# Kernel tuning notes

Measured on AMD Instinct MI355X. Metric: run time of the kernel, lower is better.

The kernel has to match this reference:

```python
import jax, jax.numpy as jnp
import numpy as np

H = 32   # hidden_size
E = 64   # embed_size
L = 3    # gru num_layers
V = 258  # vocab (256 pixel values + 2 specials)
B, C, R, S = 16, 3, 64, 64


def setup_inputs() -> dict:
    key = jax.random.key(0)
    ks = jax.random.split(key, 18)
    sc = jnp.float32(0.15)
    f = lambda k, shp: (jax.random.normal(k, shp, dtype=jnp.float32) * sc)
    return {
        "x": jax.random.randint(ks[0], (B, C, R, S), 0, V),
        "target": jax.random.randint(ks[1], (B, C, R, S), 0, V),
        "emb": f(ks[2], (3, V, E)),
        "gru_Wih0": f(ks[3], (3, 3 * H, E + 1)),
        "gru_WihR": f(ks[4], (3, L - 1, 3 * H, H)),
        "gru_Whh": f(ks[5], (3, L, 3 * H, H)),
        "gru_bih": f(ks[6], (3, L, 3 * H)),
        "gru_bhh": f(ks[7], (3, L, 3 * H)),
        "h2e_W": f(ks[8], (3, E + 1, H)),
        "h2e_b": f(ks[9], (3, E + 1)),
        "adp_W": f(ks[10], (2, E + 1, H)),
        "adp_b": f(ks[11], (2, E + 1)),
        "red_W": f(ks[12], (V, H)),
        "red_b": f(ks[13], (V,)),
        "green_W": f(ks[14], (V, H + E)),
        "green_b": f(ks[15], (V,)),
        "blue_W": f(ks[16], (V, H + 2 * E)),
        "blue_b": f(ks[17], (V,)),
    }


def _gru(comb, Wih0, WihR, Whh, bih, bhh):
    # comb: (B, S, E+1). Multi-layer GRU over the col axis, zero initial hidden.
    # PyTorch gate order: r, z, n.
    b = comb.shape[0]
    h0 = jnp.zeros((L, b, H), comb.dtype)

    def step(h, x_t):
        inp = x_t
        hs = []
        for l in range(L):
            Wih = Wih0 if l == 0 else WihR[l - 1]
            gi = inp @ Wih.T + bih[l]
            gh = h[l] @ Whh[l].T + bhh[l]
            r = jax.nn.sigmoid(gi[:, :H] + gh[:, :H])
            z = jax.nn.sigmoid(gi[:, H:2 * H] + gh[:, H:2 * H])
            n = jnp.tanh(gi[:, 2 * H:] + r * gh[:, 2 * H:])
            hl = (1.0 - z) * n + z * h[l]
            hs.append(hl)
            inp = hl
        return jnp.stack(hs), inp  # output = top-layer hidden

    _, outs = jax.lax.scan(step, h0, jnp.swapaxes(comb, 0, 1))
    return jnp.swapaxes(outs, 0, 1)  # (B, S, H)


def _forward(x, target, emb, gru_Wih0, gru_WihR, gru_Whh, gru_bih, gru_bhh,
             h2e_W, h2e_b, adp_W, adp_b, red_W, red_b, green_W, green_b,
             blue_W, blue_b):
    b, _, r_, s_ = x.shape
    row_pos = ((jnp.arange(r_) / r_) * 2.0 - 1.0).astype(jnp.float32)
    row_feat = jnp.broadcast_to(row_pos[None, :, None, None], (b, r_, s_, 1))

    outs = []
    prev = None
    for c in range(3):
        ex = jnp.concatenate([emb[c][x[:, c]], row_feat], axis=-1)  # (B,R,S,E+1)
        if c > 0:
            xs = (jnp.swapaxes(ex, 0, 1), jnp.swapaxes(prev, 0, 1))
        else:
            xs = jnp.swapaxes(ex, 0, 1)

        def row_step(ph, xr, c=c):
            # ph: (B, S, H) = GRU output of previous row
            if c > 0:
                cur, po = xr
                comb = cur + ph @ h2e_W[c].T + h2e_b[c] + po @ adp_W[c - 1].T + adp_b[c - 1]
            else:
                comb = xr + ph @ h2e_W[c].T + h2e_b[c]
            g = _gru(comb, gru_Wih0[c], gru_WihR[c], gru_Whh[c], gru_bih[c], gru_bhh[c])
            return g, g

        _, o = jax.lax.scan(row_step, jnp.zeros((b, s_, H), jnp.float32), xs)
        o = jnp.swapaxes(o, 0, 1)  # (B, R, S, H)
        outs.append(o)
        prev = o

    red_logits = outs[0] @ red_W.T + red_b
    red_e = emb[0][target[:, 0]]
    green_logits = jnp.concatenate([outs[1], red_e], axis=-1) @ green_W.T + green_b
    green_e = emb[1][target[:, 1]]
    blue_logits = jnp.concatenate([outs[2], red_e, green_e], axis=-1) @ blue_W.T + blue_b
    return jnp.stack([red_logits, green_logits, blue_logits], axis=1)  # (B,3,R,S,V)


def reference(x, target, emb, gru_Wih0, gru_WihR, gru_Whh, gru_bih, gru_bhh,
              h2e_W, h2e_b, adp_W, adp_b, red_W, red_b, green_W, green_b,
              blue_W, blue_b):
    return _forward(x, target, emb, gru_Wih0, gru_WihR, gru_Whh, gru_bih,
                    gru_bhh, h2e_W, h2e_b, adp_W, adp_b, red_W, red_b,
                    green_W, green_b, blue_W, blue_b)
```

## Files before the change

### kernel.cpp

```cpp
#include <hip/hip_runtime.h>
#include <hip/hip_bf16.h>

using bf16 = __hip_bfloat16;
typedef __attribute__((ext_vector_type(8))) short bfrag;
typedef __attribute__((ext_vector_type(4))) float ffrag;

constexpr int kH  = 32;
constexpr int kE  = 64;
constexpr int kV  = 258;
constexpr int kB  = 16;
constexpr int kR  = 64;
constexpr int kS  = 64;
constexpr int kG  = 96;
constexpr int kEP = 65;

constexpr int H2_OFF   = (3*kB*kR*kS*kH)/2;
constexpr int PROG_OFF = H2_OFF;
constexpr int T_OFF    = H2_OFF + kB*kR*kH;
constexpr int WPH_OFF  = T_OFF + 3*kV*kG;
constexpr int WADP_OFF = WPH_OFF + 3*kG*kH;
constexpr int C0_OFF   = WADP_OFF + 2*kG*kH;
constexpr int RW_OFF   = C0_OFF + 3*kG;
constexpr int TG_OFF   = RW_OFF + 3*kG;
constexpr int TBR_OFF  = TG_OFF + kV*kV;
constexpr int TBG_OFF  = TBR_OFF + kV*kV;
constexpr int P_EMB    = TBG_OFF + kV*kV;
constexpr int P_WIH0   = P_EMB    + 3*kV*kE;
constexpr int P_WIHR   = P_WIH0   + 3*kG*kEP;
constexpr int P_WHH    = P_WIHR   + 3*2*kG*kH;
constexpr int P_BIH    = P_WHH    + 3*3*kG*kH;
constexpr int P_BHH    = P_BIH    + 3*3*kG;
constexpr int P_H2EW   = P_BHH    + 3*3*kG;
constexpr int P_H2EB   = P_H2EW   + 3*kEP*kH;
constexpr int P_ADPW   = P_H2EB   + 3*kEP;
constexpr int P_ADPB   = P_ADPW   + 2*kEP*kH;
constexpr int P_REDW   = P_ADPB   + 2*kEP;
constexpr int P_REDB   = P_REDW   + kV*kH;
constexpr int P_GREENW = P_REDB   + kV;
constexpr int P_GREENB = P_GREENW + kV*(kH+kE);
constexpr int P_BLUEW  = P_GREENB + kV;
constexpr int P_BLUEB  = P_BLUEW  + kV*(kH+2*kE);
constexpr int WS_END   = P_BLUEB  + kV;

__device__ __forceinline__ float tof(bf16 h) { return __bfloat162float(h); }

__device__ __forceinline__ unsigned short bfbits(bf16 h) {
  union { bf16 h; unsigned short u; } cv; cv.h = h; return cv.u;
}
__device__ __forceinline__ short f2b(float v) {
  return (short)bfbits(__float2bfloat16(v));
}
__device__ __forceinline__ float b2f(short s) {
  union { unsigned short u; } cv; cv.u = (unsigned short)s;
  bf16 h; __builtin_memcpy(&h, &cv.u, 2); return __bfloat162float(h);
}
__device__ __forceinline__ float sigm(float v) { return 1.0f / (1.0f + __expf(-v)); }
__device__ __forceinline__ float tanh_(float v) { return 1.0f - 2.0f / (__expf(2.0f * v) + 1.0f); }

#define MFMA16(a, bb, cc) __builtin_amdgcn_mfma_f32_16x16x32_bf16((a), (bb), (cc), 0, 0, 0)

__device__ __forceinline__ void lds_barrier() {
  __builtin_amdgcn_sched_barrier(0);
  asm volatile("s_waitcnt lgkmcnt(0)" ::: "memory");
  __builtin_amdgcn_s_barrier();
  __builtin_amdgcn_sched_barrier(0);
}

__global__ void norm_kernel(const void* p0, const void* p1, const void* p2, const void* p3,
                            const void* p4, const void* p5, const void* p6, const void* p7,
                            const void* p8, const void* p9, const void* p10, const void* p11,
                            const void* p12, const void* p13, const void* p14, const void* p15,
                            float* __restrict__ wsf)
{
  constexpr int counts[16] = {3*kV*kE, 3*kG*kEP, 3*2*kG*kH, 3*3*kG*kH, 3*3*kG, 3*3*kG,
                              3*kEP*kH, 3*kEP, 2*kEP*kH, 2*kEP, kV*kH, kV,
                              kV*(kH+kE), kV, kV*(kH+2*kE), kV};
  constexpr int dsts[16] = {P_EMB, P_WIH0, P_WIHR, P_WHH, P_BIH, P_BHH,
                            P_H2EW, P_H2EB, P_ADPW, P_ADPB, P_REDW, P_REDB,
                            P_GREENW, P_GREENB, P_BLUEW, P_BLUEB};
  const void* srcs[16] = {p0,p1,p2,p3,p4,p5,p6,p7,p8,p9,p10,p11,p12,p13,p14,p15};

  __shared__ unsigned int smax;
  const int a = blockIdx.x;
  const void* src = srcs[a];
  const int n = counts[a];
  if (threadIdx.x == 0) smax = 0;
  if (a == 0) {
    int* prog = (int*)(wsf + PROG_OFF);
    for (int i = threadIdx.x; i < 48; i += 256) prog[i] = 0;
  }
  __syncthreads();

  const unsigned short* u16 = (const unsigned short*)src;
  const int ns = (n < 2048) ? n : 2048;
  unsigned int lm = 0;
  for (int i = threadIdx.x; i < ns; i += 256) {
    unsigned int e = ((unsigned int)u16[i] >> 7) & 0xFFu;
    if (e > lm) lm = e;
  }
  atomicMax(&smax, lm);
  __syncthreads();

  const bool isf32 = (smax >= 135);
  float* dst = wsf + dsts[a];
  if (isf32) {
    const float* s = (const float*)src;
    for (int i = threadIdx.x; i < n; i += 256) dst[i] = s[i];
  } else {
    const bf16* s = (const bf16*)src;
    for (int i = threadIdx.x; i < n; i += 256) dst[i] = tof(s[i]);
  }
}

__global__ void prep_kernel(float* __restrict__ wsf)
{
  int idx = blockIdx.x * 256 + threadIdx.x;

  if (idx < 3*kV*kG) {
    int c = idx / (kV*kG);
    int rem = idx - c*(kV*kG);
    int v = rem / kG;
    int j = rem - v*kG;
    const float* ev = wsf + P_EMB + (c*kV + v)*kE;
    const float* wr = wsf + P_WIH0 + (c*kG + j)*kEP;
    float acc = 0.f;
    for (int e = 0; e < kE; ++e) acc = fmaf(ev[e], wr[e], acc);
    wsf[T_OFF + idx] = acc;
    return;
  }
  idx -= 3*kV*kG;

  if (idx < 3*kG*kH) {
    int c = idx / (kG*kH);
    int rem = idx - c*(kG*kH);
    int j = rem >> 5;
    int k = rem & 31;
    const float* wr = wsf + P_WIH0 + (c*kG + j)*kEP;
    const float* hw = wsf + P_H2EW + c*kEP*kH + k;
    float acc = 0.f;
    for (int e = 0; e < kEP; ++e) acc = fmaf(wr[e], hw[e*kH], acc);
    wsf[WPH_OFF + idx] = acc;
    return;
  }
  idx -= 3*kG*kH;

  if (idx < 2*kG*kH) {
    int cm = idx / (kG*kH);
    int rem = idx - cm*(kG*kH);
    int j = rem >> 5;
    int k = rem & 31;
    const float* wr = wsf + P_WIH0 + ((cm+1)*kG + j)*kEP;
    const float* aw = wsf + P_ADPW + cm*kEP*kH + k;
    float acc = 0.f;
    for (int e = 0; e < kEP; ++e) acc = fmaf(wr[e], aw[e*kH], acc);
    wsf[WADP_OFF + idx] = acc;
    return;
  }
  idx -= 2*kG*kH;

  if (idx < 3*kG) {
    int c = idx / kG;
    int j = idx - c*kG;
    const float* wr = wsf + P_WIH0 + (c*kG + j)*kEP;
    float acc = wsf[P_BIH + (c*3 + 0)*kG + j];
    for (int e = 0; e < kEP; ++e) acc = fmaf(wsf[P_H2EB + c*kEP + e], wr[e], acc);
    if (c > 0)
      for (int e = 0; e < kEP; ++e) acc = fmaf(wsf[P_ADPB + (c-1)*kEP + e], wr[e], acc);
    wsf[C0_OFF + idx] = acc;
    return;
  }
  idx -= 3*kG;

  if (idx < 3*kG) {
    int c = idx / kG;
    int j = idx - c*kG;
    wsf[RW_OFF + idx] = wsf[P_WIH0 + (c*kG + j)*kEP + kE];
    return;
  }
  idx -= 3*kG;

  if (idx < kV*kV) {
    int v = idx / kV, w = idx - (idx / kV)*kV;
    const float* ev = wsf + P_EMB + v*kE;
    const float* gw = wsf + P_GREENW + w*(kH + kE) + kH;
    float acc = 0.f;
    for (int e = 0; e < kE; ++e) acc = fmaf(ev[e], gw[e], acc);
    wsf[TG_OFF + idx] = acc;
    return;
  }
  idx -= kV*kV;

  if (idx < kV*kV) {
    int v = idx / kV, w = idx - (idx / kV)*kV;
    const float* ev = wsf + P_EMB + v*kE;
    const float* bw = wsf + P_BLUEW + w*(kH + 2*kE) + kH;
    float acc = 0.f;
    for (int e = 0; e < kE; ++e) acc = fmaf(ev[e], bw[e], acc);
    wsf[TBR_OFF + idx] = acc;
    return;
  }
  idx -= kV*kV;

  if (idx < kV*kV) {
    int v = idx / kV, w = idx - (idx / kV)*kV;
    const float* ev = wsf + P_EMB + (kV + v)*kE;
    const float* bw = wsf + P_BLUEW + w*(kH + 2*kE) + kH + kE;
    float acc = 0.f;
    for (int e = 0; e < kE; ++e) acc = fmaf(ev[e], bw[e], acc);
    wsf[TBG_OFF + idx] = acc;
  }
}

__global__ void tfold_kernel(float* __restrict__ wsf)
{
  int idx = blockIdx.x * 256 + threadIdx.x;
  if (idx >= 3*kV*kG) return;
  int c = idx / (kV*kG);
  int g = idx % kG;
  float add = wsf[C0_OFF + c*kG + g];
  if (g < 2*kH) add += wsf[P_BHH + (c*3 + 0)*kG + g];
  wsf[T_OFF + idx] += add;
}

__global__ __launch_bounds__(256, 1)
void recur_all_kernel(const int* __restrict__ x, float* __restrict__ wsf)
{
  __shared__ __align__(16) short RING[2][kR][kH];
  __shared__ __align__(16) short H0L[kR][kH];
  __shared__ __align__(16) short H1L[kR][kH];

  const int wg = blockIdx.x;
  const int c  = wg >> 4;
  const int b  = wg & 15;
  const int tid = threadIdx.x;
  const int w    = tid >> 6;
  const int lane = tid & 63;
  const int m    = lane & 15;
  const int q    = lane >> 4;
  const int ln   = m;
  const int cb0  = w * 16;

  for (int i = tid; i < 2*kR*kH; i += 256) (&RING[0][0][0])[i] = 0;
  for (int i = tid; i < kR*kH;   i += 256) (&H0L[0][0])[i] = 0;
  for (int i = tid; i < kR*kH;   i += 256) (&H1L[0][0])[i] = 0;

  const float* wsrc[7];
  wsrc[0] = wsf + WPH_OFF + c*kG*kH;
  wsrc[1] = wsf + P_WHH  + (c*3+0)*kG*kH;
  wsrc[2] = wsf + P_WIHR + (c*2+0)*kG*kH;
  wsrc[3] = wsf + P_WHH  + (c*3+1)*kG*kH;
  wsrc[4] = wsf + P_WIHR + (c*2+1)*kG*kH;
  wsrc[5] = wsf + P_WHH  + (c*3+2)*kG*kH;
  wsrc[6] = (c > 0) ? (wsf + WADP_OFF + (c-1)*kG*kH) : (wsf + WPH_OFF);
  bfrag Wb[7][6];
#pragma unroll
  for (int mt = 0; mt < 7; ++mt) {
#pragma unroll
    for (int u = 0; u < 6; ++u) {
      const float* p = wsrc[mt] + (u*16 + ln)*kH + q*8;
#pragma unroll
      for (int j = 0; j < 8; ++j) Wb[mt][u][j] = f2b(p[j]);
    }
  }

  float rwt[6], bh0n[2], bi1z[4], bi1n[2], bh1n[2], bi2z[4], bi2n[2], bh2n[2];
#pragma unroll
  for (int u = 0; u < 6; ++u) rwt[u] = wsf[RW_OFF + c*kG + u*16 + ln];
#pragma unroll
  for (int u = 0; u < 4; ++u) {
    int g = u*16 + ln;
    bi1z[u] = wsf[P_BIH + (c*3+1)*kG + g] + wsf[P_BHH + (c*3+1)*kG + g];
    bi2z[u] = wsf[P_BIH + (c*3+2)*kG + g] + wsf[P_BHH + (c*3+2)*kG + g];
  }
#pragma unroll
  for (int t2 = 0; t2 < 2; ++t2) {
    int g = 64 + t2*16 + ln;
    bh0n[t2] = wsf[P_BHH + (c*3+0)*kG + g];
    bi1n[t2] = wsf[P_BIH + (c*3+1)*kG + g];
    bh1n[t2] = wsf[P_BHH + (c*3+1)*kG + g];
    bi2n[t2] = wsf[P_BIH + (c*3+2)*kG + g];
    bh2n[t2] = wsf[P_BHH + (c*3+2)*kG + g];
  }

  float h0s[8], h1s[8], h2s[8];
#pragma unroll
  for (int i = 0; i < 8; ++i) { h0s[i] = 0.f; h1s[i] = 0.f; h2s[i] = 0.f; }

  unsigned short* outsAll = (unsigned short*)wsf;
  unsigned short* outsC = outsAll + (size_t)(c*kB + b) * (kR*kS*kH);
  const unsigned short* outsP = outsAll + (size_t)(((c > 0 ? c : 1) - 1)*kB + b) * (kR*kS*kH);
  int* prog = (int*)(wsf + PROG_OFF);
  const int* xc = x + (b*3 + c) * kR * kS;
  const float* Tc = wsf + T_OFF + (size_t)c * kV * kG;

  int rr0[4]; float rpw[4];
#pragma unroll
  for (int i = 0; i < 4; ++i) {
    rr0[i] = cb0 + q*4 + i;
    rpw[i] = (float)rr0[i] * (2.0f/64.0f) - 1.0f;
  }

  float tv[6][4];
  bfrag poPre;
  auto load_tv = [&](int dd) {
#pragma unroll
    for (int i = 0; i < 4; ++i) {
      int sv = dd - rr0[i];
      int scl = sv < 0 ? 0 : (sv > 63 ? 63 : sv);
      int xiv = xc[rr0[i]*kS + scl];
      const float* tp = Tc + (size_t)xiv*kG;
#pragma unroll
      for (int u = 0; u < 6; ++u) tv[u][i] = tp[u*16 + ln];
    }
  };
  auto load_po = [&](int dd) {
    int sv = dd - (cb0 + m);
    int scl = sv < 0 ? 0 : (sv > 63 ? 63 : sv);
    poPre = *(const bfrag*)&outsP[((size_t)(cb0 + m)*kS + scl)*kH + q*8];
  };
  load_tv(cb0);
#pragma unroll
  for (int j = 0; j < 8; ++j) poPre[j] = 0;

  __syncthreads();

  constexpr int DELTA = 4;
  constexpr int TT = (kR + kS - 1) + 2*DELTA;
  for (int t = 0; t < TT; ++t) {
    const int d = t - c*DELTA;

    if (tid == 0) {
      if (c < 2 && d >= 1 && d <= 127)
        __hip_atomic_store(&prog[c*16 + b], d, __ATOMIC_RELEASE, __HIP_MEMORY_SCOPE_AGENT);
      if (c > 0 && d >= -1 && d <= 125) {
        const int need = d + 2;
        while (__hip_atomic_load(&prog[(c-1)*16 + b], __ATOMIC_ACQUIRE,
                                 __HIP_MEMORY_SCOPE_AGENT) < need) { }
      }
    }
    lds_barrier();

    const bool activ = (d >= cb0) && (d <= cb0 + 78);
    if (activ) {
      const int ps = (d - 1) & 1;
      const int cs = d & 1;

      int ssv[4];
      bool act[4];
#pragma unroll
      for (int i = 0; i < 4; ++i) {
        ssv[i] = d - rr0[i];
        act[i] = ((unsigned)ssv[i]) < 64u;
      }
      const int row = cb0 + m;

      bfrag phA, h0A;
      {
        int pr = row - 1;
        int prc = pr < 0 ? 0 : pr;
        phA = *(const bfrag*)&RING[ps][prc][q*8];
        if (pr < 0) {
#pragma unroll
          for (int j = 0; j < 8; ++j) phA[j] = 0;
        }
        h0A = *(const bfrag*)&H0L[row][q*8];
      }
      bfrag poA = poPre;

      ffrag rz[4], gn[2], hn[2];
#pragma unroll
      for (int u = 0; u < 4; ++u)
#pragma unroll
        for (int i = 0; i < 4; ++i) rz[u][i] = 0.f;
#pragma unroll
      for (int t2 = 0; t2 < 2; ++t2)
#pragma unroll
        for (int i = 0; i < 4; ++i) { gn[t2][i] = 0.f; hn[t2][i] = bh0n[t2]; }

#pragma unroll
      for (int u = 0; u < 4; ++u)
        rz[u] = MFMA16(phA, Wb[0][u], rz[u]);
#pragma unroll
      for (int t2 = 0; t2 < 2; ++t2)
        gn[t2] = MFMA16(phA, Wb[0][4+t2], gn[t2]);
      if (c > 0) {
#pragma unroll
        for (int u = 0; u < 4; ++u)
          rz[u] = MFMA16(poA, Wb[6][u], rz[u]);
#pragma unroll
        for (int t2 = 0; t2 < 2; ++t2)
          gn[t2] = MFMA16(poA, Wb[6][4+t2], gn[t2]);
      }
#pragma unroll
      for (int u = 0; u < 4; ++u)
        rz[u] = MFMA16(h0A, Wb[1][u], rz[u]);
#pragma unroll
      for (int t2 = 0; t2 < 2; ++t2)
        hn[t2] = MFMA16(h0A, Wb[1][4+t2], hn[t2]);

#pragma unroll
      for (int u = 0; u < 4; ++u)
#pragma unroll
        for (int i = 0; i < 4; ++i) rz[u][i] += tv[u][i] + rpw[i]*rwt[u];
#pragma unroll
      for (int t2 = 0; t2 < 2; ++t2)
#pragma unroll
        for (int i = 0; i < 4; ++i) gn[t2][i] += tv[4+t2][i] + rpw[i]*rwt[4+t2];

      if (d + 1 <= cb0 + 78) {
        load_tv(d + 1);
        if (c > 0) load_po(d + 1);
      }

#pragma unroll
      for (int i = 0; i < 4; ++i)
#pragma unroll
        for (int th = 0; th < 2; ++th) {
          float rg = sigm(rz[th][i]);
          float zg = sigm(rz[2+th][i]);
          float ng = tanh_(gn[th][i] + rg*hn[th][i]);
          float h0v = (1.f - zg)*ng + zg*h0s[i*2+th];
          if (act[i]) {
            h0s[i*2+th] = h0v;
            H0L[rr0[i]][th*16 + ln] = f2b(h0v);
          }
        }
      bfrag h0An = *(const bfrag*)&H0L[row][q*8];

      bfrag h1A = *(const bfrag*)&H1L[row][q*8];
      ffrag rz1[4], gn1[2], hn1[2];
#pragma unroll
      for (int u = 0; u < 4; ++u)
#pragma unroll
        for (int i = 0; i < 4; ++i) rz1[u][i] = bi1z[u];
#pragma unroll
      for (int t2 = 0; t2 < 2; ++t2)
#pragma unroll
        for (int i = 0; i < 4; ++i) { gn1[t2][i] = bi1n[t2]; hn1[t2][i] = bh1n[t2]; }
#pragma unroll
      for (int u = 0; u < 4; ++u) {
        rz1[u] = MFMA16(h0An, Wb[2][u], rz1[u]);
        rz1[u] = MFMA16(h1A,  Wb[3][u], rz1[u]);
      }
#pragma unroll
      for (int t2 = 0; t2 < 2; ++t2) {
        gn1[t2] = MFMA16(h0An, Wb[2][4+t2], gn1[t2]);
        hn1[t2] = MFMA16(h1A,  Wb[3][4+t2], hn1[t2]);
      }
#pragma unroll
      for (int i = 0; i < 4; ++i)
#pragma unroll
        for (int th = 0; th < 2; ++th) {
          float rg = sigm(rz1[th][i]);
          float zg = sigm(rz1[2+th][i]);
          float ng = tanh_(gn1[th][i] + rg*hn1[th][i]);
          float h1v = (1.f - zg)*ng + zg*h1s[i*2+th];
          if (act[i]) {
            h1s[i*2+th] = h1v;
            H1L[rr0[i]][th*16 + ln] = f2b(h1v);
          }
        }
      bfrag h1An = *(const bfrag*)&H1L[row][q*8];

      bfrag h2A = *(const bfrag*)&RING[ps][row][q*8];
      if (m == d - cb0) {
#pragma unroll
        for (int j = 0; j < 8; ++j) h2A[j] = 0;
      }
      ffrag rz2[4], gn2[2], hn2[2];
#pragma unroll
      for (int u = 0; u < 4; ++u)
#pragma unroll
        for (int i = 0; i < 4; ++i) rz2[u][i] = bi2z[u];
#pragma unroll
      for (int t2 = 0; t2 < 2; ++t2)
#pragma unroll
        for (int i = 0; i < 4; ++i) { gn2[t2][i] = bi2n[t2]; hn2[t2][i] = bh2n[t2]; }
#pragma unroll
      for (int u = 0; u < 4; ++u) {
        rz2[u] = MFMA16(h1An, Wb[4][u], rz2[u]);
        rz2[u] = MFMA16(h2A,  Wb[5][u], rz2[u]);
      }
#pragma unroll
      for (int t2 = 0; t2 < 2; ++t2) {
        gn2[t2] = MFMA16(h1An, Wb[4][4+t2], gn2[t2]);
        hn2[t2] = MFMA16(h2A,  Wb[5][4+t2], hn2[t2]);
      }
#pragma unroll
      for (int i = 0; i < 4; ++i)
#pragma unroll
        for (int th = 0; th < 2; ++th) {
          float rg = sigm(rz2[th][i]);
          float zg = sigm(rz2[2+th][i]);
          float ng = tanh_(gn2[th][i] + rg*hn2[th][i]);
          float h2old = (ssv[i] == 0) ? 0.f : h2s[i*2+th];
          float h2v = (1.f - zg)*ng + zg*h2old;
          if (act[i]) {
            h2s[i*2+th] = h2v;
            short hb = f2b(h2v);
            RING[cs][rr0[i]][th*16 + ln] = hb;
            outsC[((size_t)rr0[i]*kS + ssv[i])*kH + th*16 + ln] = (unsigned short)hb;
          }
        }
    } else {
      if (d + 1 >= cb0 && d + 1 <= cb0 + 78) {
        load_tv(d + 1);
        if (c > 0) load_po(d + 1);
      }
    }

    if (c < 2) {
      __builtin_amdgcn_sched_barrier(0);
      asm volatile("s_waitcnt vmcnt(0)" ::: "memory");
    }
    lds_barrier();
  }
}

__global__ __launch_bounds__(256, 1)
void logits_kernel(const int* __restrict__ target, const float* __restrict__ wsf,
                   float* __restrict__ out)
{
  const int bx = blockIdx.x;
  const int ch = bx >> 10;
  const int b  = (bx >> 6) & 15;
  const int r  = bx & 63;

  const int tid  = threadIdx.x;
  const int wave = tid >> 6;
  const int lane = tid & 63;
  const int ln   = lane & 15;
  const int q    = lane >> 4;

  const int s0  = wave * 16;
  const int rsb = r * 64 + s0;

  const unsigned short* outsAll = (const unsigned short*)wsf;
  const unsigned short* hvp = outsAll + (size_t)(ch*kB + b)*(kR*kS*kH)
                                      + (size_t)(rsb + ln)*kH + q*8;
  bfrag hvA = *(const bfrag*)hvp;

  int trv[4], tgv[4];
  if (ch >= 1) {
    const int* tgt0 = target + (b*3 + 0)*4096;
#pragma unroll
    for (int i = 0; i < 4; ++i) trv[i] = tgt0[rsb + q*4 + i];
  }
  if (ch == 2) {
    const int* tgt1 = target + (b*3 + 1)*4096;
#pragma unroll
    for (int i = 0; i < 4; ++i) tgv[i] = tgt1[rsb + q*4 + i];
  }

  const float* wbase; const float* bbase; int wstride;
  if (ch == 0)      { wbase = wsf + P_REDW;   bbase = wsf + P_REDB;   wstride = kH; }
  else if (ch == 1) { wbase = wsf + P_GREENW; bbase = wsf + P_GREENB; wstride = kH + kE; }
  else              { wbase = wsf + P_BLUEW;  bbase = wsf + P_BLUEB;  wstride = kH + 2*kE; }

  const size_t obase = ((size_t)(b*3 + ch)*4096 + rsb);
  const float* TGt  = wsf + TG_OFF;
  const float* TBRt = wsf + TBR_OFF;
  const float* TBGt = wsf + TBG_OFF;

#pragma unroll
  for (int t = 0; t < 17; ++t) {
    const int v0 = t * 16;
    const int vr = v0 + ln;
    const int vv = (vr < kV) ? vr : (kV - 1);

    bfrag whi, wlo;
    {
      const float* wrow = wbase + (size_t)vv*wstride + q*8;
#pragma unroll
      for (int j = 0; j < 8; ++j) {
        float wv = wrow[j];
        short hi = f2b(wv);
        whi[j] = hi;
        wlo[j] = f2b(wv - b2f(hi));
      }
    }

    float bias = bbase[vv];
    ffrag acc;
#pragma unroll
    for (int i = 0; i < 4; ++i) {
      float a = bias;
      if (ch == 1)      a += TGt[(size_t)trv[i]*kV + vv];
      else if (ch == 2) a += TBRt[(size_t)trv[i]*kV + vv] + TBGt[(size_t)tgv[i]*kV + vv];
      acc[i] = a;
    }

    acc = MFMA16(hvA, wlo, acc);
    acc = MFMA16(hvA, whi, acc);

    if (vr < kV) {
#pragma unroll
      for (int i = 0; i < 4; ++i)
        out[(obase + q*4 + i)*kV + vr] = acc[i];
    }
  }
}

extern "C" void kernel_launch(void* const* d_in, const int* in_sizes, int n_in,
                              void* d_out, int out_size, void* d_ws, size_t ws_size,
                              hipStream_t stream)
{
  const int* x      = (const int*)d_in[0];
  const int* target = (const int*)d_in[1];
  float* wsf = (float*)d_ws;

  norm_kernel<<<16, 256, 0, stream>>>(d_in[2], d_in[3], d_in[4], d_in[5], d_in[6], d_in[7],
                                      d_in[8], d_in[9], d_in[10], d_in[11], d_in[12], d_in[13],
                                      d_in[14], d_in[15], d_in[16], d_in[17], wsf);
  const int prepN = 3*kV*kG + 3*kG*kH + 2*kG*kH + 3*kG + 3*kG + 3*kV*kV;
  prep_kernel<<<(prepN + 255)/256, 256, 0, stream>>>(wsf);
  tfold_kernel<<<(3*kV*kG + 255)/256, 256, 0, stream>>>(wsf);
  recur_all_kernel<<<48, 256, 0, stream>>>(x, wsf);
  logits_kernel<<<3*16*64, 256, 0, stream>>>(target, wsf, (float*)d_out);
}
```

Measured before the change: 1.197 ms.

## Pack two batches per recurrent block, drop trailing barrier, pipeline prefetch, fast rcp

```diff
diff --git a/kernel.cpp b/kernel.cpp
--- a/kernel.cpp
+++ b/kernel.cpp
@@ -54,8 +54,11 @@
   union { unsigned short u; } cv; cv.u = (unsigned short)s;
   bf16 h; __builtin_memcpy(&h, &cv.u, 2); return __bfloat162float(h);
 }
-__device__ __forceinline__ float sigm(float v) { return 1.0f / (1.0f + __expf(-v)); }
-__device__ __forceinline__ float tanh_(float v) { return 1.0f - 2.0f / (__expf(2.0f * v) + 1.0f); }
+__device__ __forceinline__ float frcp(float x) {
+  float r; asm("v_rcp_f32 %0, %1" : "=v"(r) : "v"(x)); return r;
+}
+__device__ __forceinline__ float sigm(float v) { return frcp(1.0f + __expf(-v)); }
+__device__ __forceinline__ float tanh_(float v) { return 1.0f - 2.0f*frcp(__expf(2.0f*v) + 1.0f); }
 
 #define MFMA16(a, bb, cc) __builtin_amdgcn_mfma_f32_16x16x32_bf16((a), (bb), (cc), 0, 0, 0)
 
@@ -222,27 +225,30 @@
   wsf[T_OFF + idx] += add;
 }
 
-__global__ __launch_bounds__(256, 1)
+__global__ __launch_bounds__(512, 2)
 void recur_all_kernel(const int* __restrict__ x, float* __restrict__ wsf)
 {
-  __shared__ __align__(16) short RING[2][kR][kH];
-  __shared__ __align__(16) short H0L[kR][kH];
-  __shared__ __align__(16) short H1L[kR][kH];
+  __shared__ __align__(16) short RING[2][2][kR][kH];
+  __shared__ __align__(16) short H0L[2][kR][kH];
+  __shared__ __align__(16) short H1L[2][kR][kH];
 
   const int wg = blockIdx.x;
-  const int c  = wg >> 4;
-  const int b  = wg & 15;
-  const int tid = threadIdx.x;
-  const int w    = tid >> 6;
+  const int c  = wg >> 3;
+  const int p  = wg & 7;
+  const int tid  = threadIdx.x;
+  const int half = tid >> 8;
+  const int b    = p*2 + half;
+  const int t2   = tid & 255;
+  const int w    = t2 >> 6;
   const int lane = tid & 63;
   const int m    = lane & 15;
   const int q    = lane >> 4;
   const int ln   = m;
   const int cb0  = w * 16;
 
-  for (int i = tid; i < 2*kR*kH; i += 256) (&RING[0][0][0])[i] = 0;
-  for (int i = tid; i < kR*kH;   i += 256) (&H0L[0][0])[i] = 0;
-  for (int i = tid; i < kR*kH;   i += 256) (&H1L[0][0])[i] = 0;
+  for (int i = tid; i < 2*2*kR*kH; i += 512) (&RING[0][0][0][0])[i] = 0;
+  for (int i = tid; i < 2*kR*kH;   i += 512) (&H0L[0][0][0])[i] = 0;
+  for (int i = tid; i < 2*kR*kH;   i += 512) (&H1L[0][0][0])[i] = 0;
 
   const float* wsrc[7];
   wsrc[0] = wsf + WPH_OFF + c*kG*kH;
@@ -257,9 +263,9 @@
   for (int mt = 0; mt < 7; ++mt) {
 #pragma unroll
     for (int u = 0; u < 6; ++u) {
-      const float* p = wsrc[mt] + (u*16 + ln)*kH + q*8;
-#pragma unroll
-      for (int j = 0; j < 8; ++j) Wb[mt][u][j] = f2b(p[j]);
+      const float* pp = wsrc[mt] + (u*16 + ln)*kH + q*8;
+#pragma unroll
+      for (int j = 0; j < 8; ++j) Wb[mt][u][j] = f2b(pp[j]);
     }
   }
 
@@ -273,13 +279,13 @@
     bi2z[u] = wsf[P_BIH + (c*3+2)*kG + g] + wsf[P_BHH + (c*3+2)*kG + g];
   }
 #pragma unroll
-  for (int t2 = 0; t2 < 2; ++t2) {
-    int g = 64 + t2*16 + ln;
-    bh0n[t2] = wsf[P_BHH + (c*3+0)*kG + g];
-    bi1n[t2] = wsf[P_BIH + (c*3+1)*kG + g];
-    bh1n[t2] = wsf[P_BHH + (c*3+1)*kG + g];
-    bi2n[t2] = wsf[P_BIH + (c*3+2)*kG + g];
-    bh2n[t2] = wsf[P_BHH + (c*3+2)*kG + g];
+  for (int s2 = 0; s2 < 2; ++s2) {
+    int g = 64 + s2*16 + ln;
+    bh0n[s2] = wsf[P_BHH + (c*3+0)*kG + g];
+    bi1n[s2] = wsf[P_BIH + (c*3+1)*kG + g];
+    bh1n[s2] = wsf[P_BHH + (c*3+1)*kG + g];
+    bi2n[s2] = wsf[P_BIH + (c*3+2)*kG + g];
+    bh2n[s2] = wsf[P_BHH + (c*3+2)*kG + g];
   }
 
   float h0s[8], h1s[8], h2s[8];
@@ -301,26 +307,51 @@
   }
 
   float tv[6][4];
+  int   xin[4];
   bfrag poPre;
-  auto load_tv = [&](int dd) {
+  const int d0 = -c*4;
+  {
 #pragma unroll
     for (int i = 0; i < 4; ++i) {
-      int sv = dd - rr0[i];
+      int sv = d0 - rr0[i];
       int scl = sv < 0 ? 0 : (sv > 63 ? 63 : sv);
-      int xiv = xc[rr0[i]*kS + scl];
-      const float* tp = Tc + (size_t)xiv*kG;
-#pragma unroll
-      for (int u = 0; u < 6; ++u) tv[u][i] = tp[u*16 + ln];
+      xin[i] = xc[rr0[i]*kS + scl];
+    }
+#pragma unroll
+    for (int i = 0; i < 4; ++i) {
+      const float* tp = Tc + (size_t)xin[i]*kG;
+#pragma unroll
+      for (int u = 0; u < 6; ++u) tv[u][i] = tp[u*16 + ln] + rpw[i]*rwt[u];
+    }
+#pragma unroll
+    for (int i = 0; i < 4; ++i) {
+      int sv = d0 + 1 - rr0[i];
+      int scl = sv < 0 ? 0 : (sv > 63 ? 63 : sv);
+      xin[i] = xc[rr0[i]*kS + scl];
+    }
+#pragma unroll
+    for (int j = 0; j < 8; ++j) poPre[j] = 0;
+  }
+
+  auto do_prefetch = [&](int d) {
+#pragma unroll
+    for (int i = 0; i < 4; ++i) {
+      const float* tp = Tc + (size_t)xin[i]*kG;
+#pragma unroll
+      for (int u = 0; u < 6; ++u) tv[u][i] = tp[u*16 + ln] + rpw[i]*rwt[u];
+    }
+#pragma unroll
+    for (int i = 0; i < 4; ++i) {
+      int sv = d + 2 - rr0[i];
+      int scl = sv < 0 ? 0 : (sv > 63 ? 63 : sv);
+      xin[i] = xc[rr0[i]*kS + scl];
+    }
+    {
+      int sv = d + 1 - (cb0 + m);
+      int scl = sv < 0 ? 0 : (sv > 63 ? 63 : sv);
+      poPre = *(const bfrag*)&outsP[((size_t)(cb0 + m)*kS + scl)*kH + q*8];
     }
   };
-  auto load_po = [&](int dd) {
-    int sv = dd - (cb0 + m);
-    int scl = sv < 0 ? 0 : (sv > 63 ? 63 : sv);
-    poPre = *(const bfrag*)&outsP[((size_t)(cb0 + m)*kS + scl)*kH + q*8];
-  };
-  load_tv(cb0);
-#pragma unroll
-  for (int j = 0; j < 8; ++j) poPre[j] = 0;
 
   __syncthreads();
 
@@ -329,16 +360,14 @@
   for (int t = 0; t < TT; ++t) {
     const int d = t - c*DELTA;
 
-    if (tid == 0) {
-      if (c < 2 && d >= 1 && d <= 127)
-        __hip_atomic_store(&prog[c*16 + b], d, __ATOMIC_RELEASE, __HIP_MEMORY_SCOPE_AGENT);
-      if (c > 0 && d >= -1 && d <= 125) {
-        const int need = d + 2;
-        while (__hip_atomic_load(&prog[(c-1)*16 + b], __ATOMIC_ACQUIRE,
-                                 __HIP_MEMORY_SCOPE_AGENT) < need) { }
-      }
+    if (t2 == 0 && c > 0 && d >= -1 && d <= 125) {
+      const int need = d + 2;
+      while (__hip_atomic_load(&prog[(c-1)*16 + b], __ATOMIC_ACQUIRE,
+                               __HIP_MEMORY_SCOPE_AGENT) < need) { }
     }
     lds_barrier();
+    if (t2 == 0 && c < 2 && d >= 1 && d <= 127)
+      __hip_atomic_store(&prog[c*16 + b], d, __ATOMIC_RELEASE, __HIP_MEMORY_SCOPE_AGENT);
 
     const bool activ = (d >= cb0) && (d <= cb0 + 78);
     if (activ) {
@@ -358,12 +387,12 @@
       {
         int pr = row - 1;
         int prc = pr < 0 ? 0 : pr;
-        phA = *(const bfrag*)&RING[ps][prc][q*8];
+        phA = *(const bfrag*)&RING[half][ps][prc][q*8];
         if (pr < 0) {
 #pragma unroll
           for (int j = 0; j < 8; ++j) phA[j] = 0;
         }
-        h0A = *(const bfrag*)&H0L[row][q*8];
+        h0A = *(const bfrag*)&H0L[half][row][q*8];
       }
       bfrag poA = poPre;
 
@@ -373,44 +402,41 @@
 #pragma unroll
         for (int i = 0; i < 4; ++i) rz[u][i] = 0.f;
 #pragma unroll
-      for (int t2 = 0; t2 < 2; ++t2)
-#pragma unroll
-        for (int i = 0; i < 4; ++i) { gn[t2][i] = 0.f; hn[t2][i] = bh0n[t2]; }
+      for (int s2 = 0; s2 < 2; ++s2)
+#pragma unroll
+        for (int i = 0; i < 4; ++i) { gn[s2][i] = 0.f; hn[s2][i] = bh0n[s2]; }
 
 #pragma unroll
       for (int u = 0; u < 4; ++u)
         rz[u] = MFMA16(phA, Wb[0][u], rz[u]);
 #pragma unroll
-      for (int t2 = 0; t2 < 2; ++t2)
-        gn[t2] = MFMA16(phA, Wb[0][4+t2], gn[t2]);
+      for (int s2 = 0; s2 < 2; ++s2)
+        gn[s2] = MFMA16(phA, Wb[0][4+s2], gn[s2]);
       if (c > 0) {
 #pragma unroll
         for (int u = 0; u < 4; ++u)
           rz[u] = MFMA16(poA, Wb[6][u], rz[u]);
 #pragma unroll
-        for (int t2 = 0; t2 < 2; ++t2)
-          gn[t2] = MFMA16(poA, Wb[6][4+t2], gn[t2]);
+        for (int s2 = 0; s2 < 2; ++s2)
+          gn[s2] = MFMA16(poA, Wb[6][4+s2], gn[s2]);
       }
 #pragma unroll
       for (int u = 0; u < 4; ++u)
         rz[u] = MFMA16(h0A, Wb[1][u], rz[u]);
 #pragma unroll
-      for (int t2 = 0; t2 < 2; ++t2)
-        hn[t2] = MFMA16(h0A, Wb[1][4+t2], hn[t2]);
+      for (int s2 = 0; s2 < 2; ++s2)
+        hn[s2] = MFMA16(h0A, Wb[1][4+s2], hn[s2]);
 
 #pragma unroll
       for (int u = 0; u < 4; ++u)
 #pragma unroll
-        for (int i = 0; i < 4; ++i) rz[u][i] += tv[u][i] + rpw[i]*rwt[u];
-#pragma unroll
-      for (int t2 = 0; t2 < 2; ++t2)
-#pragma unroll
-        for (int i = 0; i < 4; ++i) gn[t2][i] += tv[4+t2][i] + rpw[i]*rwt[4+t2];
-
-      if (d + 1 <= cb0 + 78) {
-        load_tv(d + 1);
-        if (c > 0) load_po(d + 1);
-      }
+        for (int i = 0; i < 4; ++i) rz[u][i] += tv[u][i];
+#pragma unroll
+      for (int s2 = 0; s2 < 2; ++s2)
+#pragma unroll
+        for (int i = 0; i < 4; ++i) gn[s2][i] += tv[4+s2][i];
+
+      do_prefetch(d);
 
 #pragma unroll
       for (int i = 0; i < 4; ++i)
@@ -422,30 +448,30 @@
           float h0v = (1.f - zg)*ng + zg*h0s[i*2+th];
           if (act[i]) {
             h0s[i*2+th] = h0v;
-            H0L[rr0[i]][th*16 + ln] = f2b(h0v);
+            H0L[half][rr0[i]][th*16 + ln] = f2b(h0v);
           }
         }
-      bfrag h0An = *(const bfrag*)&H0L[row][q*8];
-
-      bfrag h1A = *(const bfrag*)&H1L[row][q*8];
+      bfrag h0An = *(const bfrag*)&H0L[half][row][q*8];
+
+      bfrag h1A = *(const bfrag*)&H1L[half][row][q*8];
       ffrag rz1[4], gn1[2], hn1[2];
 #pragma unroll
       for (int u = 0; u < 4; ++u)
 #pragma unroll
         for (int i = 0; i < 4; ++i) rz1[u][i] = bi1z[u];
 #pragma unroll
-      for (int t2 = 0; t2 < 2; ++t2)
-#pragma unroll
-        for (int i = 0; i < 4; ++i) { gn1[t2][i] = bi1n[t2]; hn1[t2][i] = bh1n[t2]; }
+      for (int s2 = 0; s2 < 2; ++s2)
+#pragma unroll
+        for (int i = 0; i < 4; ++i) { gn1[s2][i] = bi1n[s2]; hn1[s2][i] = bh1n[s2]; }
 #pragma unroll
       for (int u = 0; u < 4; ++u) {
         rz1[u] = MFMA16(h0An, Wb[2][u], rz1[u]);
         rz1[u] = MFMA16(h1A,  Wb[3][u], rz1[u]);
       }
 #pragma unroll
-      for (int t2 = 0; t2 < 2; ++t2) {
-        gn1[t2] = MFMA16(h0An, Wb[2][4+t2], gn1[t2]);
-        hn1[t2] = MFMA16(h1A,  Wb[3][4+t2], hn1[t2]);
+      for (int s2 = 0; s2 < 2; ++s2) {
+        gn1[s2] = MFMA16(h0An, Wb[2][4+s2], gn1[s2]);
+        hn1[s2] = MFMA16(h1A,  Wb[3][4+s2], hn1[s2]);
       }
 #pragma unroll
       for (int i = 0; i < 4; ++i)
@@ -457,12 +483,12 @@
           float h1v = (1.f - zg)*ng + zg*h1s[i*2+th];
           if (act[i]) {
             h1s[i*2+th] = h1v;
-            H1L[rr0[i]][th*16 + ln] = f2b(h1v);
+            H1L[half][rr0[i]][th*16 + ln] = f2b(h1v);
           }
         }
-      bfrag h1An = *(const bfrag*)&H1L[row][q*8];
-
-      bfrag h2A = *(const bfrag*)&RING[ps][row][q*8];
+      bfrag h1An = *(const bfrag*)&H1L[half][row][q*8];
+
+      bfrag h2A = *(const bfrag*)&RING[half][ps][row][q*8];
       if (m == d - cb0) {
 #pragma unroll
         for (int j = 0; j < 8; ++j) h2A[j] = 0;
@@ -473,18 +499,18 @@
 #pragma unroll
         for (int i = 0; i < 4; ++i) rz2[u][i] = bi2z[u];
 #pragma unroll
-      for (int t2 = 0; t2 < 2; ++t2)
-#pragma unroll
-        for (int i = 0; i < 4; ++i) { gn2[t2][i] = bi2n[t2]; hn2[t2][i] = bh2n[t2]; }
+      for (int s2 = 0; s2 < 2; ++s2)
+#pragma unroll
+        for (int i = 0; i < 4; ++i) { gn2[s2][i] = bi2n[s2]; hn2[s2][i] = bh2n[s2]; }
 #pragma unroll
       for (int u = 0; u < 4; ++u) {
         rz2[u] = MFMA16(h1An, Wb[4][u], rz2[u]);
         rz2[u] = MFMA16(h2A,  Wb[5][u], rz2[u]);
       }
 #pragma unroll
-      for (int t2 = 0; t2 < 2; ++t2) {
-        gn2[t2] = MFMA16(h1An, Wb[4][4+t2], gn2[t2]);
-        hn2[t2] = MFMA16(h2A,  Wb[5][4+t2], hn2[t2]);
+      for (int s2 = 0; s2 < 2; ++s2) {
+        gn2[s2] = MFMA16(h1An, Wb[4][4+s2], gn2[s2]);
+        hn2[s2] = MFMA16(h2A,  Wb[5][4+s2], hn2[s2]);
       }
 #pragma unroll
       for (int i = 0; i < 4; ++i)
@@ -498,22 +524,18 @@
           if (act[i]) {
             h2s[i*2+th] = h2v;
             short hb = f2b(h2v);
-            RING[cs][rr0[i]][th*16 + ln] = hb;
+            RING[half][cs][rr0[i]][th*16 + ln] = hb;
             outsC[((size_t)rr0[i]*kS + ssv[i])*kH + th*16 + ln] = (unsigned short)hb;
           }
         }
     } else {
-      if (d + 1 >= cb0 && d + 1 <= cb0 + 78) {
-        load_tv(d + 1);
-        if (c > 0) load_po(d + 1);
-      }
+      do_prefetch(d);
     }
 
     if (c < 2) {
       __builtin_amdgcn_sched_barrier(0);
       asm volatile("s_waitcnt vmcnt(0)" ::: "memory");
     }
-    lds_barrier();
   }
 }
 
@@ -615,6 +637,6 @@
   const int prepN = 3*kV*kG + 3*kG*kH + 2*kG*kH + 3*kG + 3*kG + 3*kV*kV;
   prep_kernel<<<(prepN + 255)/256, 256, 0, stream>>>(wsf);
   tfold_kernel<<<(3*kV*kG + 255)/256, 256, 0, stream>>>(wsf);
-  recur_all_kernel<<<48, 256, 0, stream>>>(x, wsf);
+  recur_all_kernel<<<24, 512, 0, stream>>>(x, wsf);
   logits_kernel<<<3*16*64, 256, 0, stream>>>(target, wsf, (float*)d_out);
 }
```

Measured after the change: 1.698 ms. 41.8% more time.
